# Performance work log

Measured on AMD Instinct MI355X. Metric: run time of the kernel, lower is better.

Reference implementation:

```python
import jax, jax.numpy as jnp
import numpy as np

B, S, P, H = 4, 4096, 2048, 4096


def setup_inputs() -> dict:
    key = jax.random.key(0)
    k1, k2 = jax.random.split(key)
    word_embeddings = jax.random.normal(k1, (B, S, H), dtype=jnp.float32)
    patch_embeddings = jax.random.normal(k2, (B, P, H), dtype=jnp.float32)
    # First P sequence positions are image-patch placeholders holding indices
    # 0..P-1 into patch_embeddings; the remaining positions are -1 (text tokens).
    row = jnp.concatenate([jnp.arange(P, dtype=jnp.int32),
                           -jnp.ones((S - P,), dtype=jnp.int32)])
    image_patches_indices = jnp.broadcast_to(row, (B, S))
    return {
        "word_embeddings": word_embeddings,
        "patch_embeddings": patch_embeddings,
        "image_patches_indices": image_patches_indices,
    }


def reference(word_embeddings, patch_embeddings, image_patches_indices):
    # Vectorized equivalent of the per-batch nonzero+gather+scatter loop:
    # for every position with index >= 0, replace the word embedding with the
    # corresponding row of patch_embeddings; otherwise keep the word embedding.
    mask = image_patches_indices >= 0                       # [B, S]
    src = jnp.maximum(image_patches_indices, 0)             # clamp -1 -> 0 (masked out)
    gathered = jnp.take_along_axis(patch_embeddings, src[..., None], axis=1)  # [B, S, H]
    return jnp.where(mask[..., None], gathered, word_embeddings)
```

## Files before the change

kernel.cpp:

```cpp
#include <hip/hip_runtime.h>


#define BB 4
#define SS 4096
#define PP 2048
#define HH 4096

__global__ __launch_bounds__(256) void CombineEmbeddings_50319836840460_kernel(
    const float4* __restrict__ word,
    const float4* __restrict__ patch,
    const int*    __restrict__ idx,
    float4*       __restrict__ out)
{
    const int Hv = HH / 4;
    long long t = (long long)blockIdx.x * blockDim.x + threadIdx.x;
    int row = (int)(t >> 10);
    int col = (int)(t & (Hv - 1));
    int b   = row >> 12;

    int id = idx[row];
    float4 v;
    if (id >= 0) {
        v = patch[((long long)b * PP + id) * Hv + col];
    } else {
        v = word[t];
    }
    out[t] = v;
}

extern "C" void kernel_launch(void* const* d_in, const int* in_sizes, int n_in,
                              void* d_out, int out_size, void* d_ws, size_t ws_size,
                              hipStream_t stream) {
    const float4* word  = (const float4*)d_in[0];
    const float4* patch = (const float4*)d_in[1];
    const int*    idx   = (const int*)d_in[2];
    float4*       out   = (float4*)d_out;

    const long long total_vec = (long long)BB * SS * (HH / 4);
    const int block = 256;
    const int grid  = (int)(total_vec / block);

    CombineEmbeddings_50319836840460_kernel<<<grid, block, 0, stream>>>(
        word, patch, idx, out);
}
```

Measured before the change: 467.6 us.

## Process one row per block with four vector loads and nontemporal stores

Each block now handles one full embedding row. It reads the index once, picks the source row pointer, and issues four float4 loads per thread before writing them back with nontemporal stores. This removes per-thread index loads and branch divergence, gives more memory-level parallelism per thread, and keeps output writes from polluting the cache. Offsets now use 32-bit int arithmetic, which still fits the fixed sizes.

```diff
diff --git a/kernel.cpp b/kernel.cpp
--- a/kernel.cpp
+++ b/kernel.cpp
@@ -6,39 +6,48 @@
 #define PP 2048
 #define HH 4096
 
+typedef float f4 __attribute__((ext_vector_type(4)));
+
 __global__ __launch_bounds__(256) void CombineEmbeddings_50319836840460_kernel(
-    const float4* __restrict__ word,
-    const float4* __restrict__ patch,
-    const int*    __restrict__ idx,
-    float4*       __restrict__ out)
+    const f4* __restrict__ word,
+    const f4* __restrict__ patch,
+    const int* __restrict__ idx,
+    f4*       __restrict__ out)
 {
-    const int Hv = HH / 4;
-    long long t = (long long)blockIdx.x * blockDim.x + threadIdx.x;
-    int row = (int)(t >> 10);
-    int col = (int)(t & (Hv - 1));
-    int b   = row >> 12;
+    constexpr int Hv = HH / 4;
 
-    int id = idx[row];
-    float4 v;
-    if (id >= 0) {
-        v = patch[((long long)b * PP + id) * Hv + col];
-    } else {
-        v = word[t];
-    }
-    out[t] = v;
+    const int row = blockIdx.x;
+    const int b   = row >> 12;
+    const int id  = idx[row];
+
+    const f4* __restrict__ src = (id >= 0)
+        ? patch + (b * PP + id) * Hv
+        : word  + row * Hv;
+    f4* __restrict__ dst = out + row * Hv;
+
+    const int c = threadIdx.x;
+
+    f4 v0 = src[c];
+    f4 v1 = src[c + 256];
+    f4 v2 = src[c + 512];
+    f4 v3 = src[c + 768];
+
+    __builtin_nontemporal_store(v0, &dst[c]);
+    __builtin_nontemporal_store(v1, &dst[c + 256]);
+    __builtin_nontemporal_store(v2, &dst[c + 512]);
+    __builtin_nontemporal_store(v3, &dst[c + 768]);
 }
 
 extern "C" void kernel_launch(void* const* d_in, const int* in_sizes, int n_in,
                               void* d_out, int out_size, void* d_ws, size_t ws_size,
                               hipStream_t stream) {
-    const float4* word  = (const float4*)d_in[0];
-    const float4* patch = (const float4*)d_in[1];
-    const int*    idx   = (const int*)d_in[2];
-    float4*       out   = (float4*)d_out;
+    const f4* word  = (const f4*)d_in[0];
+    const f4* patch = (const f4*)d_in[1];
+    const int* idx  = (const int*)d_in[2];
+    f4*       out   = (f4*)d_out;
 
-    const long long total_vec = (long long)BB * SS * (HH / 4);
+    const int grid  = BB * SS;
     const int block = 256;
-    const int grid  = (int)(total_vec / block);
 
     CombineEmbeddings_50319836840460_kernel<<<grid, block, 0, stream>>>(
         word, patch, idx, out);
```

Result: slower. 494.4 us (+5.7%).
